# Performance work log

Measured on AMD Instinct MI355X. Metric: run time of the kernel, lower is better.

The kernel has to match this reference:

```python
import jax, jax.numpy as jnp
import numpy as np

DIM = 192
WS = 8
HEADS = 6
HD = DIM // HEADS
RECON_W = 0.1
EPS = 1e-6


def setup_inputs() -> dict:
    key = jax.random.key(0)
    ks = jax.random.split(key, 10)
    d = DIM

    def rn(k, shape, scale=0.02):
        return jax.random.normal(k, shape, jnp.float32) * scale

    return {
        "x": jax.random.normal(ks[0], (4, d, 224, 224), jnp.float32),
        "w_pre1": rn(ks[1], (d, d)), "b_pre1": jnp.zeros((d,), jnp.float32),
        "w_dw": rn(ks[2], (d, 3, 3)), "b_dw": jnp.zeros((d,), jnp.float32),
        "ln_g": jnp.ones((d,), jnp.float32), "ln_b": jnp.zeros((d,), jnp.float32),
        "w_qkv": rn(ks[3], (d, 3 * d)), "b_qkv": jnp.zeros((3 * d,), jnp.float32),
        "w_proj": rn(ks[4], (d, d)), "b_proj": jnp.zeros((d,), jnp.float32),
        "w_g1": rn(ks[5], (d, 4 * d)), "b_g1": jnp.zeros((4 * d,), jnp.float32),
        "w_g2": rn(ks[6], (4 * d, d)), "b_g2": jnp.zeros((d,), jnp.float32),
        "w_rec": rn(ks[7], (d, d)), "b_rec": jnp.zeros((d,), jnp.float32),
    }


def _forward(x, w_pre1, b_pre1, w_dw, b_dw, ln_g, ln_b, w_qkv, b_qkv,
             w_proj, b_proj, w_g1, b_g1, w_g2, b_g2, w_rec, b_rec):
    B, C, H, W = x.shape
    ws, nh, hd = WS, HEADS, HD
    shortcut = x

    # preprocess: 1x1 conv then depthwise 3x3 conv (padding=1)
    f = jnp.einsum('bchw,oc->bohw', x, w_pre1) + b_pre1[None, :, None, None]
    f = jax.lax.conv_general_dilated(
        f, w_dw[:, None, :, :], (1, 1), 'SAME',
        feature_group_count=C,
        dimension_numbers=('NCHW', 'OIHW', 'NCHW')) + b_dw[None, :, None, None]

    # LayerNorm2d: LN over channel dim
    f = f.transpose(0, 2, 3, 1)  # BHWC
    mu = f.mean(-1, keepdims=True)
    var = f.var(-1, keepdims=True)
    f = (f - mu) / jnp.sqrt(var + EPS) * ln_g + ln_b

    # window partition (H, W divisible by ws -> no padding needed)
    nH, nW = H // ws, W // ws
    p = f.reshape(B, nH, ws, nW, ws, C).transpose(0, 1, 3, 2, 4, 5)
    p = p.reshape(B * nH * nW, ws * ws, C)  # [N, T, C]
    N, T, _ = p.shape

    # qkv + windowed multi-head attention
    qkv = p @ w_qkv + b_qkv
    q, k, v = jnp.split(qkv, 3, axis=-1)
    qh = q.reshape(N, T, nh, hd)
    kh = k.reshape(N, T, nh, hd)
    vh = v.reshape(N, T, nh, hd)
    scale = hd ** (-0.5)
    attn = jnp.einsum('nqhd,nkhd->nhqk', qh, kh) * scale
    attn = jax.nn.softmax(attn, axis=-1)
    out_attn = jnp.einsum('nhqk,nkhd->nqhd', attn, vh).reshape(N, T, C)

    # GMLP on v (dropout is identity in eval); torch GELU is exact erf form
    g = jax.nn.gelu(v @ w_g1 + b_g1, approximate=False) @ w_g2 + b_g2

    fused = (out_attn * g) @ w_proj + b_proj

    # recon head + L1 loss vs detached window tokens
    recon = fused @ w_rec + b_rec
    recon_loss = jnp.mean(jnp.abs(recon - jax.lax.stop_gradient(p))) * RECON_W

    # window reverse
    out = fused.reshape(B, nH, nW, ws, ws, C).transpose(0, 5, 1, 3, 2, 4)
    out = out.reshape(B, C, H, W)
    return out + shortcut, recon_loss


def reference(x, w_pre1, b_pre1, w_dw, b_dw, ln_g, ln_b, w_qkv, b_qkv,
              w_proj, b_proj, w_g1, b_g1, w_g2, b_g2, w_rec, b_rec):
    return _forward(x, w_pre1, b_pre1, w_dw, b_dw, ln_g, ln_b, w_qkv, b_qkv,
                    w_proj, b_proj, w_g1, b_g1, w_g2, b_g2, w_rec, b_rec)
```

## Files before the change

### kernel.cpp

```cpp
#include <hip/hip_runtime.h>
#include <hip/hip_bf16.h>
#include <math.h>

#define BATCH 4
#define CDIM 192
#define HDIM 224
#define WDIM 224
#define HWSZ (HDIM * WDIM)
#define NWH 28
#define NWIN (BATCH * NWH * NWH)
#define TOK 64
#define MTOK (NWIN * TOK)
#define HEADS 6
#define C3 (3 * CDIM)
#define C4 (4 * CDIM)
#define IMGSZ (BATCH * CDIM * HWSZ)
#define ATTN_SCALE 0.17677669529663687f
#define LN_EPS 1e-6f
#define PBP 200

typedef __attribute__((ext_vector_type(8))) short bfrag;
typedef __attribute__((ext_vector_type(4))) float f32x4;

__device__ __forceinline__ float bf2f(unsigned short u) {
    union { unsigned int i; float f; } v; v.i = ((unsigned int)u) << 16; return v.f;
}
__device__ __forceinline__ unsigned short f2bf(float f) {
    union { unsigned int i; float f; } v; v.f = f;
    unsigned int r = (v.i + 0x7FFFu + ((v.i >> 16) & 1u)) >> 16;
    return (unsigned short)r;
}
__device__ __forceinline__ float gelu_erf(float x) {
    float z = fabsf(x) * 0.70710678118654752f;
    float t = __fdividef(1.0f, 1.0f + 0.3275911f * z);
    float poly = t * (0.254829592f + t * (-0.284496736f +
                 t * (1.421413741f + t * (-1.453152027f + t * 1.061405429f))));
    float erfv = 1.0f - poly * __expf(-z * z);
    erfv = (x < 0.f) ? -erfv : erfv;
    return 0.5f * x * (1.0f + erfv);
}
__device__ __forceinline__ void gload16(void* lds, const void* g) {
    __builtin_amdgcn_global_load_lds(
        (const __attribute__((address_space(1))) void*)g,
        (__attribute__((address_space(3))) void*)lds, 16, 0, 0);
}

__launch_bounds__(256)
__global__ void prep_weights_kernel(const float* __restrict__ w_qkv,
                                    const float* __restrict__ w_g1,
                                    const float* __restrict__ w_g2,
                                    const float* __restrict__ w_proj,
                                    const float* __restrict__ w_rec,
                                    ushort* __restrict__ WqkvT,
                                    ushort* __restrict__ W1T,
                                    ushort* __restrict__ W2C,
                                    ushort* __restrict__ WpT,
                                    ushort* __restrict__ WrT) {
    int idx = blockIdx.x * 256 + threadIdx.x;
    if (idx < 576 * 192) {
        int n = idx / 192, k = idx % 192;
        WqkvT[idx] = f2bf(w_qkv[(size_t)k * C3 + n]);
    }
    if (idx < 768 * 192) {
        int n = idx / 192, k = idx % 192;
        W1T[idx] = f2bf(w_g1[(size_t)k * C4 + n]);
    }
    if (idx < 192 * 768) {
        int hc = idx / 12288, rem = idx % 12288;
        int n = rem / 64, kloc = rem & 63;
        W2C[idx] = f2bf(w_g2[(size_t)(hc * 64 + kloc) * CDIM + n]);
    }
    if (idx < 192 * 192) {
        int n = idx / 192, k = idx % 192;
        WpT[idx] = f2bf(w_proj[(size_t)k * CDIM + n]);
        WrT[idx] = f2bf(w_rec[(size_t)k * CDIM + n]);
    }
}

__launch_bounds__(256)
__global__ void conv1x1_kernel(const float* __restrict__ x,
                               const float* __restrict__ w1,
                               const float* __restrict__ b1,
                               float* __restrict__ f1) {
    __shared__ __align__(16) float As[16][68];
    __shared__ __align__(16) float Bs[16][64];
    const int tid = threadIdx.x;
    const int p0 = blockIdx.x * 64;
    const int m0 = blockIdx.y * 64;
    const int b  = blockIdx.z;
    const int tm = tid >> 4, tn = tid & 15;
    const int mload = tid >> 2, kload = (tid & 3) * 4;
    const int kw = tid >> 4, nw = (tid & 15) * 4;
    float acc[4][4] = {};
    const float* xb = x + (size_t)b * CDIM * HWSZ;
    for (int k0 = 0; k0 < CDIM; k0 += 16) {
        float4 av = *(const float4*)&w1[(size_t)(m0 + mload) * CDIM + k0 + kload];
        float4 bv = *(const float4*)&xb[(size_t)(k0 + kw) * HWSZ + p0 + nw];
        __syncthreads();
        As[kload + 0][mload] = av.x;
        As[kload + 1][mload] = av.y;
        As[kload + 2][mload] = av.z;
        As[kload + 3][mload] = av.w;
        *(float4*)&Bs[kw][nw] = bv;
        __syncthreads();
#pragma unroll
        for (int kk = 0; kk < 16; ++kk) {
            float a[4], bb[4];
            *(float4*)a  = *(const float4*)&As[kk][tm * 4];
            *(float4*)bb = *(const float4*)&Bs[kk][tn * 4];
#pragma unroll
            for (int i = 0; i < 4; ++i)
#pragma unroll
                for (int j = 0; j < 4; ++j) acc[i][j] += a[i] * bb[j];
        }
    }
    float* outb = f1 + (size_t)b * CDIM * HWSZ;
#pragma unroll
    for (int i = 0; i < 4; ++i) {
        int m = m0 + tm * 4 + i;
        float bias = b1[m];
        float4 o = make_float4(acc[i][0] + bias, acc[i][1] + bias,
                               acc[i][2] + bias, acc[i][3] + bias);
        *(float4*)&outb[(size_t)m * HWSZ + p0 + tn * 4] = o;
    }
}

__launch_bounds__(256)
__global__ void dwconv_kernel(const float* __restrict__ f1,
                              const float* __restrict__ w_dw,
                              const float* __restrict__ b_dw,
                              float* __restrict__ f2) {
    unsigned int idx = blockIdx.x * 256u + threadIdx.x;
    int w = idx % WDIM;
    unsigned int r = idx / WDIM;
    int h = r % HDIM;
    unsigned int bc = r / HDIM;
    int c = bc % CDIM;
    const float* base = f1 + (size_t)bc * HWSZ;
    const float* wd = w_dw + c * 9;
    float acc = b_dw[c];
#pragma unroll
    for (int ky = 0; ky < 3; ++ky) {
        int hy = h + ky - 1;
        if (hy < 0 || hy >= HDIM) continue;
#pragma unroll
        for (int kx = 0; kx < 3; ++kx) {
            int wx = w + kx - 1;
            if (wx < 0 || wx >= WDIM) continue;
            acc += base[hy * WDIM + wx] * wd[ky * 3 + kx];
        }
    }
    f2[idx] = acc;
}

__launch_bounds__(256)
__global__ void ln_part_kernel(const float* __restrict__ f2,
                               const float* __restrict__ ln_g,
                               const float* __restrict__ ln_b,
                               ushort* __restrict__ pb) {
    __shared__ float T[CDIM][33];
    __shared__ float Rs[8][32], Rs2[8][32];
    __shared__ float Mu[32], Rsig[32];
    const int tid = threadIdx.x;
    const int wt = blockIdx.x, h = blockIdx.y, b = blockIdx.z;
    const int w0 = wt * 32;
    const size_t rowbase = (size_t)b * CDIM * HWSZ + (size_t)h * WDIM + w0;
    for (int idx = tid; idx < CDIM * 32; idx += 256) {
        int c = idx >> 5, j = idx & 31;
        T[c][j] = f2[rowbase + (size_t)c * HWSZ + j];
    }
    __syncthreads();
    {
        int j = tid & 31, q = tid >> 5;
        float s = 0.f, s2 = 0.f;
#pragma unroll
        for (int i = 0; i < 24; ++i) {
            float v = T[q * 24 + i][j];
            s += v; s2 += v * v;
        }
        Rs[q][j] = s; Rs2[q][j] = s2;
    }
    __syncthreads();
    if (tid < 32) {
        float s = 0.f, s2 = 0.f;
#pragma unroll
        for (int q = 0; q < 8; ++q) { s += Rs[q][tid]; s2 += Rs2[q][tid]; }
        float mu = s * (1.0f / CDIM);
        float var = s2 * (1.0f / CDIM) - mu * mu;
        Mu[tid] = mu;
        Rsig[tid] = rsqrtf(var + LN_EPS);
    }
    __syncthreads();
    const int l = tid & 63;
    const int jo = tid >> 6;
    for (int it = 0; it < 8; ++it) {
        int j = it * 4 + jo;
        int w = w0 + j;
        size_t token = ((size_t)(b * NWH + (h >> 3)) * NWH + (w >> 3)) * TOK
                       + ((h & 7) * 8 + (w & 7));
        float mu = Mu[j], rs = Rsig[j];
#pragma unroll
        for (int rep = 0; rep < 3; ++rep) {
            int c = l + rep * 64;
            pb[token * PBP + c] = f2bf((T[c][j] - mu) * rs * ln_g[c] + ln_b[c]);
        }
    }
}

__launch_bounds__(256)
__global__ void mega_kernel(const ushort* __restrict__ pb,
                            const ushort* __restrict__ WqkvT,
                            const float* __restrict__ b_qkv,
                            const ushort* __restrict__ W1T,
                            const float* __restrict__ b_g1,
                            const ushort* __restrict__ W2C,
                            const float* __restrict__ b_g2,
                            const ushort* __restrict__ WpT,
                            const float* __restrict__ b_proj,
                            const ushort* __restrict__ WrT,
                            const float* __restrict__ b_rec,
                            float* __restrict__ Fout,
                            float* __restrict__ loss) {
    __shared__ __align__(16) ushort Ab[64 * PBP];
    __shared__ __align__(16) ushort Blob[16896];
    __shared__ float red[256];
    ushort* Qb  = Blob;
    ushort* Kb  = Blob + 2560;
    ushort* Vt  = Blob + 5120;
    ushort* Pbf = Blob + 7424;
    ushort* Wb  = Blob;
    ushort* Hb  = Blob + 12288;

    const int tid = threadIdx.x;
    const int lane = tid & 63, wave = tid >> 6;
    const int quad = lane >> 4, l16 = lane & 15;
    const int m0 = wave * 16;
    const int sw = (l16 & 7) << 3;
    const size_t tok0 = (size_t)blockIdx.x * 64;

    int srcA[6], srcB[6], dst6[6];
#pragma unroll
    for (int c = 0; c < 6; ++c) {
        int P = (wave * 6 + c) * 1024 + lane * 16;
        dst6[c] = (wave * 6 + c) * 1024;
        int rA = P / 384;
        int mA = P - rA * 384;
        srcA[c] = rA * 384 + (mA ^ ((rA & 7) << 4));
        srcB[c] = P ^ (((P >> 7) & 7) << 4);
    }
    char* WbB = (char*)Wb;
    char* AbB = (char*)Ab;

#define ISSUE_W(SRC, OFFS)                                                    \
    _Pragma("unroll")                                                         \
    for (int c = 0; c < 6; ++c)                                               \
        gload16(WbB + dst6[c], (const char*)(SRC) + OFFS[c]);
#define COMPUTE_K192(ACC, BASEI)                                              \
    _Pragma("unroll")                                                         \
    for (int kk = 0; kk < 6; ++kk) {                                          \
        bfrag a = *(const bfrag*)&Ab[(m0 + l16) * PBP + kk * 32 + quad * 8];  \
        _Pragma("unroll")                                                     \
        for (int t = 0; t < 4; ++t) {                                         \
            bfrag b = *(const bfrag*)&Wb[(t * 16 + l16) * 192                 \
                                         + ((kk * 32 + quad * 8) ^ sw)];      \
            ACC[(BASEI) + t] = __builtin_amdgcn_mfma_f32_16x16x32_bf16(       \
                a, b, ACC[(BASEI) + t], 0, 0, 0);                             \
        }                                                                     \
    }

    {
        const char* src = (const char*)(pb + tok0 * PBP);
#pragma unroll
        for (int c = 0; c < 6; ++c)
            gload16(AbB + dst6[c], src + dst6[c] + lane * 16);
        if (wave == 0) gload16(AbB + 24576, src + 24576 + lane * 16);
    }
    __syncthreads();

    f32x4 oacc[12];
#pragma unroll
    for (int i = 0; i < 12; ++i) oacc[i] = (f32x4){0.f, 0.f, 0.f, 0.f};
    unsigned int vpk[12][2];

#pragma unroll
    for (int h = 0; h < HEADS; ++h) {
        const ushort* baseQ = WqkvT + (size_t)(h * 32) * 192;
        const ushort* baseK = WqkvT + (size_t)(192 + h * 32) * 192;
        const ushort* baseV = WqkvT + (size_t)(384 + h * 32) * 192;
        f32x4 acc[6];
#pragma unroll
        for (int t = 0; t < 6; ++t) acc[t] = (f32x4){0.f, 0.f, 0.f, 0.f};
#pragma unroll
        for (int kk = 0; kk < 6; ++kk) {
            const int ko = kk * 32 + quad * 8;
            bfrag b0 = *(const bfrag*)&baseQ[(size_t)l16 * 192 + ko];
            bfrag b1 = *(const bfrag*)&baseQ[(size_t)(16 + l16) * 192 + ko];
            bfrag b2 = *(const bfrag*)&baseK[(size_t)l16 * 192 + ko];
            bfrag b3 = *(const bfrag*)&baseK[(size_t)(16 + l16) * 192 + ko];
            bfrag b4 = *(const bfrag*)&baseV[(size_t)l16 * 192 + ko];
            bfrag b5 = *(const bfrag*)&baseV[(size_t)(16 + l16) * 192 + ko];
            bfrag a  = *(const bfrag*)&Ab[(m0 + l16) * PBP + ko];
            __builtin_amdgcn_s_setprio(1);
            acc[0] = __builtin_amdgcn_mfma_f32_16x16x32_bf16(a, b0, acc[0], 0, 0, 0);
            acc[1] = __builtin_amdgcn_mfma_f32_16x16x32_bf16(a, b1, acc[1], 0, 0, 0);
            acc[2] = __builtin_amdgcn_mfma_f32_16x16x32_bf16(a, b2, acc[2], 0, 0, 0);
            acc[3] = __builtin_amdgcn_mfma_f32_16x16x32_bf16(a, b3, acc[3], 0, 0, 0);
            acc[4] = __builtin_amdgcn_mfma_f32_16x16x32_bf16(a, b4, acc[4], 0, 0, 0);
            acc[5] = __builtin_amdgcn_mfma_f32_16x16x32_bf16(a, b5, acc[5], 0, 0, 0);
            __builtin_amdgcn_s_setprio(0);
        }
#pragma unroll
        for (int t = 0; t < 2; ++t) {
            float bq = b_qkv[h * 32 + t * 16 + l16];
            float bk = b_qkv[192 + h * 32 + t * 16 + l16];
            float bv = b_qkv[384 + h * 32 + t * 16 + l16];
            ushort vb[4];
#pragma unroll
            for (int reg = 0; reg < 4; ++reg) {
                int row = m0 + quad * 4 + reg;
                Qb[row * 40 + t * 16 + l16] = f2bf((acc[t][reg] + bq) * ATTN_SCALE);
                Kb[row * 40 + t * 16 + l16] = f2bf(acc[t + 2][reg] + bk);
                ushort vv = f2bf(acc[t + 4][reg] + bv);
                Vt[(t * 16 + l16) * 72 + row] = vv;
                vb[reg] = vv;
            }
            vpk[h * 2 + t][0] = (unsigned int)vb[0] | ((unsigned int)vb[1] << 16);
            vpk[h * 2 + t][1] = (unsigned int)vb[2] | ((unsigned int)vb[3] << 16);
        }
        __syncthreads();

        f32x4 s[4];
        {
            bfrag aq = *(const bfrag*)&Qb[(m0 + l16) * 40 + quad * 8];
            bfrag k0 = *(const bfrag*)&Kb[(l16) * 40 + quad * 8];
            bfrag k1 = *(const bfrag*)&Kb[(16 + l16) * 40 + quad * 8];
            bfrag k2 = *(const bfrag*)&Kb[(32 + l16) * 40 + quad * 8];
            bfrag k3 = *(const bfrag*)&Kb[(48 + l16) * 40 + quad * 8];
            __builtin_amdgcn_s_setprio(1);
            s[0] = __builtin_amdgcn_mfma_f32_16x16x32_bf16(
                aq, k0, (f32x4){0.f, 0.f, 0.f, 0.f}, 0, 0, 0);
            s[1] = __builtin_amdgcn_mfma_f32_16x16x32_bf16(
                aq, k1, (f32x4){0.f, 0.f, 0.f, 0.f}, 0, 0, 0);
            s[2] = __builtin_amdgcn_mfma_f32_16x16x32_bf16(
                aq, k2, (f32x4){0.f, 0.f, 0.f, 0.f}, 0, 0, 0);
            s[3] = __builtin_amdgcn_mfma_f32_16x16x32_bf16(
                aq, k3, (f32x4){0.f, 0.f, 0.f, 0.f}, 0, 0, 0);
            __builtin_amdgcn_s_setprio(0);
        }
#pragma unroll
        for (int reg = 0; reg < 4; ++reg) {
            float mx = fmaxf(fmaxf(s[0][reg], s[1][reg]), fmaxf(s[2][reg], s[3][reg]));
            mx = fmaxf(mx, __shfl_xor(mx, 1));
            mx = fmaxf(mx, __shfl_xor(mx, 2));
            mx = fmaxf(mx, __shfl_xor(mx, 4));
            mx = fmaxf(mx, __shfl_xor(mx, 8));
            float e[4], sum = 0.f;
#pragma unroll
            for (int t = 0; t < 4; ++t) { e[t] = __expf(s[t][reg] - mx); sum += e[t]; }
            sum += __shfl_xor(sum, 1);
            sum += __shfl_xor(sum, 2);
            sum += __shfl_xor(sum, 4);
            sum += __shfl_xor(sum, 8);
            float inv = 1.0f / sum;
            int row = m0 + quad * 4 + reg;
#pragma unroll
            for (int t = 0; t < 4; ++t)
                Pbf[row * 72 + t * 16 + l16] = f2bf(e[t] * inv);
        }
        __syncthreads();

#pragma unroll
        for (int kk = 0; kk < 2; ++kk) {
            bfrag a  = *(const bfrag*)&Pbf[(m0 + l16) * 72 + kk * 32 + quad * 8];
            bfrag v0 = *(const bfrag*)&Vt[(l16) * 72 + kk * 32 + quad * 8];
            bfrag v1 = *(const bfrag*)&Vt[(16 + l16) * 72 + kk * 32 + quad * 8];
            __builtin_amdgcn_s_setprio(1);
            oacc[h * 2 + 0] = __builtin_amdgcn_mfma_f32_16x16x32_bf16(
                a, v0, oacc[h * 2 + 0], 0, 0, 0);
            oacc[h * 2 + 1] = __builtin_amdgcn_mfma_f32_16x16x32_bf16(
                a, v1, oacc[h * 2 + 1], 0, 0, 0);
            __builtin_amdgcn_s_setprio(0);
        }
        __syncthreads();
    }

#pragma unroll
    for (int i = 0; i < 12; ++i) {
        int n = i * 16 + l16;
        Ab[(m0 + quad * 4 + 0) * PBP + n] = (ushort)(vpk[i][0] & 0xFFFF);
        Ab[(m0 + quad * 4 + 1) * PBP + n] = (ushort)(vpk[i][0] >> 16);
        Ab[(m0 + quad * 4 + 2) * PBP + n] = (ushort)(vpk[i][1] & 0xFFFF);
        Ab[(m0 + quad * 4 + 3) * PBP + n] = (ushort)(vpk[i][1] >> 16);
    }
    ISSUE_W(W1T, srcA);
    __syncthreads();

    f32x4 acc2[12];
#pragma unroll
    for (int i = 0; i < 12; ++i) acc2[i] = (f32x4){0.f, 0.f, 0.f, 0.f};
    for (int hc = 0; hc < 12; ++hc) {
        f32x4 acc1[4];
#pragma unroll
        for (int t = 0; t < 4; ++t) acc1[t] = (f32x4){0.f, 0.f, 0.f, 0.f};
        COMPUTE_K192(acc1, 0);
#pragma unroll
        for (int t = 0; t < 4; ++t) {
            int n = t * 16 + l16;
            float bb = b_g1[hc * 64 + n];
#pragma unroll
            for (int reg = 0; reg < 4; ++reg) {
                float xv = acc1[t][reg] + bb;
                Hb[(m0 + quad * 4 + reg) * 72 + n] = f2bf(gelu_erf(xv));
            }
        }
        __syncthreads();
        ISSUE_W((const char*)W2C + (size_t)hc * 24576, srcB);
        __syncthreads();
#pragma unroll
        for (int kk = 0; kk < 2; ++kk) {
            bfrag a = *(const bfrag*)&Hb[(m0 + l16) * 72 + kk * 32 + quad * 8];
#pragma unroll
            for (int t = 0; t < 12; ++t) {
                bfrag b = *(const bfrag*)&Wb[(t * 16 + l16) * 64
                                             + ((kk * 32 + quad * 8) ^ sw)];
                acc2[t] = __builtin_amdgcn_mfma_f32_16x16x32_bf16(a, b, acc2[t], 0, 0, 0);
            }
        }
        if (hc < 11) {
            __syncthreads();
            ISSUE_W((const char*)W1T + (size_t)(hc + 1) * 24576, srcA);
            __syncthreads();
        }
    }
#pragma unroll
    for (int t = 0; t < 12; ++t) {
        int c = t * 16 + l16;
        float bg = b_g2[c];
#pragma unroll
        for (int reg = 0; reg < 4; ++reg) {
            int r = m0 + quad * 4 + reg;
            Ab[r * PBP + c] = f2bf(oacc[t][reg] * (acc2[t][reg] + bg));
        }
    }
    __syncthreads();
    ISSUE_W(WpT, srcA);
    __syncthreads();

    f32x4 facc[12];
#pragma unroll
    for (int i = 0; i < 12; ++i) facc[i] = (f32x4){0.f, 0.f, 0.f, 0.f};
    COMPUTE_K192(facc, 0);
    __syncthreads();
    ISSUE_W((const char*)WpT + 24576, srcA);
    __syncthreads();
    COMPUTE_K192(facc, 4);
    __syncthreads();
    ISSUE_W((const char*)WpT + 49152, srcA);
    __syncthreads();
    COMPUTE_K192(facc, 8);
#pragma unroll
    for (int i = 0; i < 12; ++i) {
        int n = i * 16 + l16;
        float bp = b_proj[n];
#pragma unroll
        for (int reg = 0; reg < 4; ++reg) {
            int r = m0 + quad * 4 + reg;
            float fv = facc[i][reg] + bp;
            Fout[(tok0 + r) * (size_t)CDIM + n] = fv;
            Ab[r * PBP + n] = f2bf(fv);
        }
    }
    __syncthreads();
    ISSUE_W(WrT, srcA);
    __syncthreads();

    f32x4 racc[12];
#pragma unroll
    for (int i = 0; i < 12; ++i) racc[i] = (f32x4){0.f, 0.f, 0.f, 0.f};
    COMPUTE_K192(racc, 0);
    __syncthreads();
    ISSUE_W((const char*)WrT + 24576, srcA);
    __syncthreads();
    COMPUTE_K192(racc, 4);
    __syncthreads();
    ISSUE_W((const char*)WrT + 49152, srcA);
    __syncthreads();
    COMPUTE_K192(racc, 8);

    float ls = 0.f;
#pragma unroll
    for (int i = 0; i < 12; ++i) {
        int n = i * 16 + l16;
        float br = b_rec[n];
#pragma unroll
        for (int reg = 0; reg < 4; ++reg) {
            int r = m0 + quad * 4 + reg;
            float rv = racc[i][reg] + br;
            ls += fabsf(rv - bf2f(pb[(tok0 + r) * PBP + n]));
        }
    }
    red[tid] = ls;
    __syncthreads();
    for (int s = 128; s > 0; s >>= 1) {
        if (tid < s) red[tid] += red[tid + s];
        __syncthreads();
    }
    if (tid == 0) atomicAdd(loss, red[0] * (0.1f / (float)IMGSZ));
#undef ISSUE_W
#undef COMPUTE_K192
}

__launch_bounds__(256)
__global__ void reverse_res_kernel(const float* __restrict__ fused,
                                   const float* __restrict__ x,
                                   float* __restrict__ out) {
    __shared__ float T[CDIM][33];
    const int tid = threadIdx.x;
    const int wt = blockIdx.x, h = blockIdx.y, b = blockIdx.z;
    const int w0 = wt * 32;
    const int l = tid & 63, jo = tid >> 6;
    for (int it = 0; it < 8; ++it) {
        int j = it * 4 + jo;
        int w = w0 + j;
        size_t token = ((size_t)(b * NWH + (h >> 3)) * NWH + (w >> 3)) * TOK
                       + ((h & 7) * 8 + (w & 7));
#pragma unroll
        for (int rep = 0; rep < 3; ++rep) {
            int c = l + rep * 64;
            T[c][j] = fused[token * CDIM + c];
        }
    }
    __syncthreads();
    const size_t rowbase = (size_t)b * CDIM * HWSZ + (size_t)h * WDIM + w0;
    for (int idx = tid; idx < CDIM * 32; idx += 256) {
        int c = idx >> 5, j = idx & 31;
        size_t gp = rowbase + (size_t)c * HWSZ + j;
        out[gp] = T[c][j] + x[gp];
    }
}

extern "C" void kernel_launch(void* const* d_in, const int* in_sizes, int n_in,
                              void* d_out, int out_size, void* d_ws, size_t ws_size,
                              hipStream_t stream) {
    const float* x      = (const float*)d_in[0];
    const float* w_pre1 = (const float*)d_in[1];
    const float* b_pre1 = (const float*)d_in[2];
    const float* w_dw   = (const float*)d_in[3];
    const float* b_dw   = (const float*)d_in[4];
    const float* ln_g   = (const float*)d_in[5];
    const float* ln_b   = (const float*)d_in[6];
    const float* w_qkv  = (const float*)d_in[7];
    const float* b_qkv  = (const float*)d_in[8];
    const float* w_proj = (const float*)d_in[9];
    const float* b_proj = (const float*)d_in[10];
    const float* w_g1   = (const float*)d_in[11];
    const float* b_g1   = (const float*)d_in[12];
    const float* w_g2   = (const float*)d_in[13];
    const float* b_g2   = (const float*)d_in[14];
    const float* w_rec  = (const float*)d_in[15];
    const float* b_rec  = (const float*)d_in[16];

    float* OutR = (float*)d_out;
    float* loss = OutR + (size_t)IMGSZ;
    float* A    = (float*)d_ws;

    ushort* pb    = (ushort*)d_out;
    ushort* WqkvT = pb    + (size_t)MTOK * PBP;
    ushort* W1T   = WqkvT + 576 * 192;
    ushort* W2C   = W1T   + 768 * 192;
    ushort* WpT   = W2C   + 192 * 768;
    ushort* WrT   = WpT   + 192 * 192;

    hipMemsetAsync(loss, 0, sizeof(float), stream);

    conv1x1_kernel<<<dim3(HWSZ / 64, CDIM / 64, BATCH), 256, 0, stream>>>(
        x, w_pre1, b_pre1, OutR);
    dwconv_kernel<<<IMGSZ / 256, 256, 0, stream>>>(OutR, w_dw, b_dw, A);
    prep_weights_kernel<<<(768 * 192 + 255) / 256, 256, 0, stream>>>(
        w_qkv, w_g1, w_g2, w_proj, w_rec, WqkvT, W1T, W2C, WpT, WrT);
    ln_part_kernel<<<dim3(WDIM / 32, HDIM, BATCH), 256, 0, stream>>>(
        A, ln_g, ln_b, pb);
    mega_kernel<<<NWIN, 256, 0, stream>>>(
        pb, WqkvT, b_qkv, W1T, b_g1, W2C, b_g2, WpT, b_proj, WrT, b_rec,
        A, loss);
    reverse_res_kernel<<<dim3(WDIM / 32, HDIM, BATCH), 256, 0, stream>>>(
        A, x, OutR);
}
```

Baseline: 1.541 ms.

## Halve weight staging buffer to fit three blocks per CU in mega_kernel

Shrinks the shared weight tile from 24KB to 12KB chunks, so each GEMM stage loads weights in half-size pieces, and moves the GELU hidden buffer to overlap. LDS per block falls from about 59KB to about 50KB and launch bounds request 3 blocks per CU, aiming to raise occupancy for latency hiding. In exchange the kernel issues twice as many weight load rounds and roughly twice as many __syncthreads barriers, and register pressure is constrained by the occupancy hint.

```diff
diff --git a/kernel.cpp b/kernel.cpp
--- a/kernel.cpp
+++ b/kernel.cpp
@@ -207,7 +207,7 @@
     }
 }
 
-__launch_bounds__(256)
+__launch_bounds__(256, 3)
 __global__ void mega_kernel(const ushort* __restrict__ pb,
                             const ushort* __restrict__ WqkvT,
                             const float* __restrict__ b_qkv,
@@ -222,14 +222,14 @@
                             float* __restrict__ Fout,
                             float* __restrict__ loss) {
     __shared__ __align__(16) ushort Ab[64 * PBP];
-    __shared__ __align__(16) ushort Blob[16896];
+    __shared__ __align__(16) ushort Blob[12032];
     __shared__ float red[256];
     ushort* Qb  = Blob;
     ushort* Kb  = Blob + 2560;
     ushort* Vt  = Blob + 5120;
     ushort* Pbf = Blob + 7424;
     ushort* Wb  = Blob;
-    ushort* Hb  = Blob + 12288;
+    ushort* Hb  = Blob + 6144;
 
     const int tid = threadIdx.x;
     const int lane = tid & 63, wave = tid >> 6;
@@ -238,41 +238,55 @@
     const int sw = (l16 & 7) << 3;
     const size_t tok0 = (size_t)blockIdx.x * 64;
 
-    int srcA[6], srcB[6], dst6[6];
-#pragma unroll
-    for (int c = 0; c < 6; ++c) {
-        int P = (wave * 6 + c) * 1024 + lane * 16;
-        dst6[c] = (wave * 6 + c) * 1024;
+    int srcA3[3], srcB3[3], dst3[3];
+#pragma unroll
+    for (int c = 0; c < 3; ++c) {
+        int P = (wave * 3 + c) * 1024 + lane * 16;
+        dst3[c] = (wave * 3 + c) * 1024;
         int rA = P / 384;
         int mA = P - rA * 384;
-        srcA[c] = rA * 384 + (mA ^ ((rA & 7) << 4));
-        srcB[c] = P ^ (((P >> 7) & 7) << 4);
+        srcA3[c] = rA * 384 + (mA ^ ((rA & 7) << 4));
+        srcB3[c] = P ^ (((P >> 7) & 7) << 4);
     }
     char* WbB = (char*)Wb;
     char* AbB = (char*)Ab;
 
-#define ISSUE_W(SRC, OFFS)                                                    \
+#define ISSUE_W3(SRC, OFFS)                                                   \
     _Pragma("unroll")                                                         \
-    for (int c = 0; c < 6; ++c)                                               \
-        gload16(WbB + dst6[c], (const char*)(SRC) + OFFS[c]);
-#define COMPUTE_K192(ACC, BASEI)                                              \
+    for (int c = 0; c < 3; ++c)                                               \
+        gload16(WbB + dst3[c], (const char*)(SRC) + OFFS[c]);
+#define G1_TILES(ACC, BASEI)                                                  \
     _Pragma("unroll")                                                         \
     for (int kk = 0; kk < 6; ++kk) {                                          \
         bfrag a = *(const bfrag*)&Ab[(m0 + l16) * PBP + kk * 32 + quad * 8];  \
         _Pragma("unroll")                                                     \
-        for (int t = 0; t < 4; ++t) {                                         \
+        for (int t = 0; t < 2; ++t) {                                         \
             bfrag b = *(const bfrag*)&Wb[(t * 16 + l16) * 192                 \
                                          + ((kk * 32 + quad * 8) ^ sw)];      \
             ACC[(BASEI) + t] = __builtin_amdgcn_mfma_f32_16x16x32_bf16(       \
                 a, b, ACC[(BASEI) + t], 0, 0, 0);                             \
         }                                                                     \
     }
+#define G2_HALF(S)                                                            \
+    _Pragma("unroll")                                                         \
+    for (int kk = 0; kk < 2; ++kk) {                                          \
+        bfrag a = *(const bfrag*)&Hb[(m0 + l16) * 72 + kk * 32 + quad * 8];   \
+        _Pragma("unroll")                                                     \
+        for (int t = 0; t < 6; ++t) {                                         \
+            bfrag b = *(const bfrag*)&Wb[(t * 16 + l16) * 64                  \
+                                         + ((kk * 32 + quad * 8) ^ sw)];      \
+            acc2[(S) * 6 + t] = __builtin_amdgcn_mfma_f32_16x16x32_bf16(      \
+                a, b, acc2[(S) * 6 + t], 0, 0, 0);                            \
+        }                                                                     \
+    }
 
     {
         const char* src = (const char*)(pb + tok0 * PBP);
 #pragma unroll
-        for (int c = 0; c < 6; ++c)
-            gload16(AbB + dst6[c], src + dst6[c] + lane * 16);
+        for (int c = 0; c < 6; ++c) {
+            int base = (wave * 6 + c) * 1024;
+            gload16(AbB + base, src + base + lane * 16);
+        }
         if (wave == 0) gload16(AbB + 24576, src + 24576 + lane * 16);
     }
     __syncthreads();
@@ -392,7 +406,7 @@
         Ab[(m0 + quad * 4 + 2) * PBP + n] = (ushort)(vpk[i][1] & 0xFFFF);
         Ab[(m0 + quad * 4 + 3) * PBP + n] = (ushort)(vpk[i][1] >> 16);
     }
-    ISSUE_W(W1T, srcA);
+    ISSUE_W3(W1T, srcA3);
     __syncthreads();
 
     f32x4 acc2[12];
@@ -402,7 +416,11 @@
         f32x4 acc1[4];
 #pragma unroll
         for (int t = 0; t < 4; ++t) acc1[t] = (f32x4){0.f, 0.f, 0.f, 0.f};
-        COMPUTE_K192(acc1, 0);
+        G1_TILES(acc1, 0);
+        __syncthreads();
+        ISSUE_W3((const char*)W1T + (size_t)hc * 24576 + 12288, srcA3);
+        __syncthreads();
+        G1_TILES(acc1, 2);
 #pragma unroll
         for (int t = 0; t < 4; ++t) {
             int n = t * 16 + l16;
@@ -414,21 +432,16 @@
             }
         }
         __syncthreads();
-        ISSUE_W((const char*)W2C + (size_t)hc * 24576, srcB);
-        __syncthreads();
-#pragma unroll
-        for (int kk = 0; kk < 2; ++kk) {
-            bfrag a = *(const bfrag*)&Hb[(m0 + l16) * 72 + kk * 32 + quad * 8];
-#pragma unroll
-            for (int t = 0; t < 12; ++t) {
-                bfrag b = *(const bfrag*)&Wb[(t * 16 + l16) * 64
-                                             + ((kk * 32 + quad * 8) ^ sw)];
-                acc2[t] = __builtin_amdgcn_mfma_f32_16x16x32_bf16(a, b, acc2[t], 0, 0, 0);
-            }
-        }
+        ISSUE_W3((const char*)W2C + (size_t)hc * 24576, srcB3);
+        __syncthreads();
+        G2_HALF(0);
+        __syncthreads();
+        ISSUE_W3((const char*)W2C + (size_t)hc * 24576 + 12288, srcB3);
+        __syncthreads();
+        G2_HALF(1);
         if (hc < 11) {
             __syncthreads();
-            ISSUE_W((const char*)W1T + (size_t)(hc + 1) * 24576, srcA);
+            ISSUE_W3((const char*)W1T + (size_t)(hc + 1) * 24576, srcA3);
             __syncthreads();
         }
     }
@@ -443,21 +456,21 @@
         }
     }
     __syncthreads();
-    ISSUE_W(WpT, srcA);
+    ISSUE_W3(WpT, srcA3);
     __syncthreads();
 
     f32x4 facc[12];
 #pragma unroll
     for (int i = 0; i < 12; ++i) facc[i] = (f32x4){0.f, 0.f, 0.f, 0.f};
-    COMPUTE_K192(facc, 0);
-    __syncthreads();
-    ISSUE_W((const char*)WpT + 24576, srcA);
-    __syncthreads();
-    COMPUTE_K192(facc, 4);
-    __syncthreads();
-    ISSUE_W((const char*)WpT + 49152, srcA);
-    __syncthreads();
-    COMPUTE_K192(facc, 8);
+#pragma unroll
+    for (int c = 0; c < 6; ++c) {
+        G1_TILES(facc, c * 2);
+        if (c < 5) {
+            __syncthreads();
+            ISSUE_W3((const char*)WpT + (size_t)(c + 1) * 12288, srcA3);
+            __syncthreads();
+        }
+    }
 #pragma unroll
     for (int i = 0; i < 12; ++i) {
         int n = i * 16 + l16;
@@ -471,21 +484,21 @@
         }
     }
     __syncthreads();
-    ISSUE_W(WrT, srcA);
+    ISSUE_W3(WrT, srcA3);
     __syncthreads();
 
     f32x4 racc[12];
 #pragma unroll
     for (int i = 0; i < 12; ++i) racc[i] = (f32x4){0.f, 0.f, 0.f, 0.f};
-    COMPUTE_K192(racc, 0);
-    __syncthreads();
-    ISSUE_W((const char*)WrT + 24576, srcA);
-    __syncthreads();
-    COMPUTE_K192(racc, 4);
-    __syncthreads();
-    ISSUE_W((const char*)WrT + 49152, srcA);
-    __syncthreads();
-    COMPUTE_K192(racc, 8);
+#pragma unroll
+    for (int c = 0; c < 6; ++c) {
+        G1_TILES(racc, c * 2);
+        if (c < 5) {
+            __syncthreads();
+            ISSUE_W3((const char*)WrT + (size_t)(c + 1) * 12288, srcA3);
+            __syncthreads();
+        }
+    }
 
     float ls = 0.f;
 #pragma unroll
@@ -506,8 +519,9 @@
         __syncthreads();
     }
     if (tid == 0) atomicAdd(loss, red[0] * (0.1f / (float)IMGSZ));
-#undef ISSUE_W
-#undef COMPUTE_K192
+#undef ISSUE_W3
+#undef G1_TILES
+#undef G2_HALF
 }
 
 __launch_bounds__(256)
```

Result: faster. 1.427 ms (-7.4%).
